# Optimization experiments

Hardware: AMD Instinct MI355X
Metric: run time of the kernel (lower is better)

## Reference

```python
import jax, jax.numpy as jnp
import numpy as np

B = 131072    # batch of toy 2D points
H = 256       # effective hidden width (dims[1], = out_dims * group_card)
NB = 8        # n_blocks i-ResBlocks
NMID = 3      # middle layers: dims 2->256->256->256->256->2 => 1 in + 3 mid + 1 out
NPS = 5       # n_power_series terms for log-det trace estimator


def setup_inputs() -> dict:
    key = jax.random.key(0)
    ks = jax.random.split(key, 8)
    # small scales keep each g-net contractive (coeff<1 Lipschitz, as spectral norm would)
    x  = jax.random.normal(ks[0], (B, 2), jnp.float32)
    v  = jax.random.normal(ks[1], (B, 2), jnp.float32)  # Hutchinson probe (n_samples=1)
    Wi = jax.random.normal(ks[2], (NB, 2, H), jnp.float32) * 0.05
    bi = jax.random.normal(ks[3], (NB, H), jnp.float32) * 0.01
    Wm = jax.random.normal(ks[4], (NB, NMID, H, H), jnp.float32) * (0.05 / np.sqrt(H))
    bm = jax.random.normal(ks[5], (NB, NMID, H), jnp.float32) * 0.01
    Wo = jax.random.normal(ks[6], (NB, H, 2), jnp.float32) * (0.05 / np.sqrt(H))
    bo = jax.random.normal(ks[7], (NB, 2), jnp.float32) * 0.01
    return {"x": x, "v": v, "Wi": Wi, "bi": bi, "Wm": Wm, "bm": bm, "Wo": Wo, "bo": bo}


def _g(x, Wi, bi, Wm, bm, Wo, bo):
    # equivariant 3x3 convs on 1x1 spatial maps == channel-mixing linears;
    # build_nnet appends the activation after EVERY conv, including the last.
    h = jax.nn.relu(x @ Wi + bi)
    for j in range(Wm.shape[0]):
        h = jax.nn.relu(h @ Wm[j] + bm[j])
    return jax.nn.relu(h @ Wo + bo)


def _iresblock(x, v, Wi, bi, Wm, bm, Wo, bo):
    gfun = lambda xx: _g(xx, Wi, bi, Wm, bm, Wo, bo)
    gx = gfun(x)
    # log det(I + J_g) ~= sum_{k=1..n} (-1)^{k+1}/k * v^T J_g^k v  (power series, Hutchinson)
    w = v
    logdet = jnp.zeros((x.shape[0], 1), x.dtype)
    for k in range(1, NPS + 1):
        _, w = jax.jvp(gfun, (x,), (w,))          # w <- J_g @ w
        coef = ((-1.0) ** (k + 1)) / k
        logdet = logdet + coef * jnp.sum(w * v, axis=1, keepdims=True)
    return x + gx, logdet


def reference(x, v, Wi, bi, Wm, bm, Wo, bo):
    z = x
    delta_logp = jnp.zeros((x.shape[0], 1), x.dtype)  # SequentialFlow: logpx - logdet per block
    for b in range(NB):
        z, ld = _iresblock(z, v, Wi[b], bi[b], Wm[b], bm[b], Wo[b], bo[b])
        delta_logp = delta_logp - ld
    return z, delta_logp
```

## Files before the change

### kernel.cpp

```cpp
#include <hip/hip_runtime.h>
#include <hip/hip_bf16.h>

#define BATCH 131072
#define H 256
#define NBLK 8
#define NMID 3
#define MS 16
#define RT_N 3
#define NT 256
#define CT_N 4

typedef __attribute__((ext_vector_type(8))) short short8;
typedef __attribute__((ext_vector_type(4))) float f32x4;

__device__ __forceinline__ unsigned pk2(float a, float b) {
    unsigned ua = __float_as_uint(a) + 0x8000u;
    unsigned ub = __float_as_uint(b) + 0x8000u;
    return __builtin_amdgcn_perm(ub, ua, 0x07060302u);
}

__global__ void pack_w_kernel(const float* __restrict__ Wm, unsigned short* __restrict__ Wp) {
    int o = blockIdx.x * blockDim.x + threadIdx.x;
    if (o >= NBLK * NMID * 8192) return;
    int lane  = o & 63;
    int T     = (o >> 6) & 15;
    int kk    = (o >> 10) & 7;
    int layer = o >> 13;
    int n  = (T >> 2) * 64 + (T & 1) * 32 + (lane & 15) * 2 + ((T >> 1) & 1);
    int k0 = kk * 32 + (lane >> 4) * 8;
    const float* src = Wm + (size_t)layer * H * H;
    unsigned int w[4];
    #pragma unroll
    for (int jj = 0; jj < 4; ++jj)
        w[jj] = pk2(src[(size_t)(k0 + 2*jj) * H + n], src[(size_t)(k0 + 2*jj + 1) * H + n]);
    uint4 val; val.x = w[0]; val.y = w[1]; val.z = w[2]; val.w = w[3];
    ((uint4*)Wp)[o] = val;
}

struct Packs { unsigned ph[4][2]; unsigned pa[4][2]; unsigned pb[4][2]; };

__device__ __forceinline__ void epi_compute(const f32x4 (&acc)[RT_N][CT_N],
                                            const float2 bvA, const float2 bvB, Packs& p) {
    #pragma unroll
    for (int r = 0; r < 4; ++r) {
        float a0 = acc[0][0][r] + bvA.x, a1 = acc[0][2][r] + bvA.y;
        float b0 = acc[0][1][r] + bvB.x, b1 = acc[0][3][r] + bvB.y;
        bool ma0 = a0 > 0.f, ma1 = a1 > 0.f, mb0 = b0 > 0.f, mb1 = b1 > 0.f;
        p.ph[r][0] = pk2(ma0 ? a0 : 0.f,            ma1 ? a1 : 0.f);
        p.ph[r][1] = pk2(mb0 ? b0 : 0.f,            mb1 ? b1 : 0.f);
        p.pa[r][0] = pk2(ma0 ? acc[1][0][r] : 0.f,  ma1 ? acc[1][2][r] : 0.f);
        p.pa[r][1] = pk2(mb0 ? acc[1][1][r] : 0.f,  mb1 ? acc[1][3][r] : 0.f);
        p.pb[r][0] = pk2(ma0 ? acc[2][0][r] : 0.f,  ma1 ? acc[2][2][r] : 0.f);
        p.pb[r][1] = pk2(mb0 ? acc[2][1][r] : 0.f,  mb1 ? acc[2][3][r] : 0.f);
    }
}

__device__ __forceinline__ void epi_store(const Packs& p, unsigned short* __restrict__ Xs,
                                          int wave, int lane) {
    const int mcol = lane & 15, quad = lane >> 4;
    const int qx = mcol >> 2;
    const int jb = (mcol & 3) * 2;
    const int kkA = wave * 2;
    #pragma unroll
    for (int r = 0; r < 4; ++r) {
        int le  = qx * 16 + quad * 4 + r;
        int scl = le ^ ((le >> 3) & 7);
        int e0  = kkA * 512 + scl * 8 + jb;
        *(unsigned*)(Xs + e0)               = p.ph[r][0];
        *(unsigned*)(Xs + e0 + 512)         = p.ph[r][1];
        *(unsigned*)(Xs + e0 + 4096)        = p.pa[r][0];
        *(unsigned*)(Xs + e0 + 4096 + 512)  = p.pa[r][1];
        *(unsigned*)(Xs + e0 + 8192)        = p.pb[r][0];
        *(unsigned*)(Xs + e0 + 8192 + 512)  = p.pb[r][1];
    }
}

__global__ __launch_bounds__(NT, 3)
void flow_kernel(const float* __restrict__ x, const float* __restrict__ v,
                 const float* __restrict__ Wi, const float* __restrict__ bi,
                 const float* __restrict__ bm, const float* __restrict__ Wo,
                 const float* __restrict__ bo,
                 const unsigned short* __restrict__ Wp,
                 float* __restrict__ out)
{
    __shared__ uint4 Xl4[RT_N * 8 * 64];
    __shared__ float zbuf[MS * 2];
    __shared__ float vbuf[MS * 2];

    unsigned short* Xs = (unsigned short*)Xl4;

    const int tid  = threadIdx.x;
    const int wave = tid >> 6;
    const int lane = tid & 63;
    const int mcol = lane & 15;
    const int quad = lane >> 4;
    const int s0   = blockIdx.x * MS;
    const int rl   = lane ^ ((lane >> 3) & 7);

    float dlp = 0.0f;
    if (tid < MS) {
        zbuf[tid*2+0] = x[(size_t)(s0+tid)*2+0];
        zbuf[tid*2+1] = x[(size_t)(s0+tid)*2+1];
        vbuf[tid*2+0] = v[(size_t)(s0+tid)*2+0];
        vbuf[tid*2+1] = v[(size_t)(s0+tid)*2+1];
    }
    __syncthreads();

    const int cA = wave * 64 + mcol * 2;

    for (int b = 0; b < NBLK; ++b) {
        {
            const float* Wi0 = Wi + (size_t)b * 2 * H;
            const float* Wi1 = Wi0 + H;
            short8 b0[CT_N];
            #pragma unroll
            for (int ct = 0; ct < CT_N; ++ct) {
                short8 z = {0,0,0,0,0,0,0,0};
                if (quad == 0) {
                    int n = cA + (ct & 1) * 32 + (ct >> 1);
                    unsigned p = pk2(Wi0[n], Wi1[n]);
                    z[0] = (short)(p & 0xFFFFu);
                    z[1] = (short)(p >> 16);
                }
                b0[ct] = z;
            }
            f32x4 acc[RT_N][CT_N];
            #pragma unroll
            for (int st = 0; st < RT_N; ++st)
                #pragma unroll
                for (int ct = 0; ct < CT_N; ++ct)
                    acc[st][ct] = (f32x4){0.f, 0.f, 0.f, 0.f};
            #pragma unroll
            for (int st = 0; st < RT_N; ++st) {
                short8 af = {0,0,0,0,0,0,0,0};
                if (quad == 0) {
                    if (st == 0) {
                        unsigned p = pk2(zbuf[mcol*2+0], zbuf[mcol*2+1]);
                        af[0] = (short)(p & 0xFFFFu);
                        af[1] = (short)(p >> 16);
                    } else if (st == 1) af[0] = (short)0x3F80;
                    else                af[1] = (short)0x3F80;
                }
                #pragma unroll
                for (int ct = 0; ct < CT_N; ++ct)
                    acc[st][ct] = __builtin_amdgcn_mfma_f32_16x16x32_bf16(af, b0[ct], acc[st][ct], 0, 0, 0);
            }
            Packs p;
            const float* bib = bi + (size_t)b * H;
            epi_compute(acc, *(const float2*)(bib + cA), *(const float2*)(bib + cA + 32), p);
            epi_store(p, Xs, wave, lane);
            __syncthreads();
        }

        for (int li = 0; li < NMID; ++li) {
            const int layer = b * NMID + li;
            const short8* Bp = ((const short8*)Wp) + (size_t)layer * 8192;

            f32x4 acc[RT_N][CT_N];
            #pragma unroll
            for (int st = 0; st < RT_N; ++st)
                #pragma unroll
                for (int ct = 0; ct < CT_N; ++ct)
                    acc[st][ct] = (f32x4){0.f, 0.f, 0.f, 0.f};

            #pragma unroll
            for (int kk = 0; kk < 8; ++kk) {
                short8 bf[CT_N];
                #pragma unroll
                for (int ct = 0; ct < CT_N; ++ct)
                    bf[ct] = Bp[(kk*16 + wave*4 + ct)*64 + lane];
                #pragma unroll
                for (int st = 0; st < RT_N; ++st) {
                    short8 af = ((const short8*)Xl4)[(st*8 + kk)*64 + rl];
                    #pragma unroll
                    for (int ct = 0; ct < CT_N; ++ct)
                        acc[st][ct] = __builtin_amdgcn_mfma_f32_16x16x32_bf16(af, bf[ct], acc[st][ct], 0, 0, 0);
                }
            }
            Packs p;
            const float* bmb = bm + (size_t)layer * H;
            epi_compute(acc, *(const float2*)(bmb + cA), *(const float2*)(bmb + cA + 32), p);
            __syncthreads();
            epi_store(p, Xs, wave, lane);
            __syncthreads();
        }

        {
            const float* Wob = Wo + (size_t)b * H * 2;
            const float* bob = bo + (size_t)b * 2;
            short8 b4[2];
            #pragma unroll
            for (int kki = 0; kki < 2; ++kki) {
                short8 z = {0,0,0,0,0,0,0,0};
                if (mcol < 2) {
                    int kb = (wave * 2 + kki) * 32 + quad * 8;
                    #pragma unroll
                    for (int jj = 0; jj < 4; ++jj) {
                        unsigned p = pk2(Wob[(kb + 2*jj) * 2 + mcol], Wob[(kb + 2*jj + 1) * 2 + mcol]);
                        z[2*jj]   = (short)(p & 0xFFFFu);
                        z[2*jj+1] = (short)(p >> 16);
                    }
                }
                b4[kki] = z;
            }
            f32x4 accL[RT_N];
            #pragma unroll
            for (int st = 0; st < RT_N; ++st) accL[st] = (f32x4){0.f, 0.f, 0.f, 0.f};
            #pragma unroll
            for (int st = 0; st < RT_N; ++st) {
                #pragma unroll
                for (int kki = 0; kki < 2; ++kki) {
                    short8 af = ((const short8*)Xl4)[(st*8 + wave*2 + kki)*64 + rl];
                    accL[st] = __builtin_amdgcn_mfma_f32_16x16x32_bf16(af, b4[kki], accL[st], 0, 0, 0);
                }
            }
            __syncthreads();
            float* part = (float*)Xl4;
            if (mcol < 2) {
                #pragma unroll
                for (int st = 0; st < RT_N; ++st)
                    #pragma unroll
                    for (int r = 0; r < 4; ++r)
                        part[((st*16 + quad*4 + r)*2 + mcol)*4 + wave] = accL[st][r];
            }
            __syncthreads();
            float* res = part + 384;
            if (tid < 96) {
                float4 p4 = ((const float4*)part)[tid];
                res[tid] = p4.x + p4.y + p4.z + p4.w;
            }
            __syncthreads();
            if (tid < MS) {
                float SH0 = res[tid*2],      SH1 = res[tid*2+1];
                float SA0 = res[32 + tid*2], SA1 = res[33 + tid*2];
                float SB0 = res[64 + tid*2], SB1 = res[65 + tid*2];
                float pre0 = SH0 + bob[0], pre1 = SH1 + bob[1];
                bool  m0 = pre0 > 0.f,     m1 = pre1 > 0.f;
                float gx0 = m0 ? pre0 : 0.f, gx1 = m1 ? pre1 : 0.f;
                float J00 = m0 ? SA0 : 0.f;
                float J01 = m0 ? SB0 : 0.f;
                float J10 = m1 ? SA1 : 0.f;
                float J11 = m1 ? SB1 : 0.f;
                float v0 = vbuf[tid*2+0], v1 = vbuf[tid*2+1];
                float w0 = v0, w1 = v1, ld = 0.f;
                const float coef[5] = {1.f, -0.5f, 1.f/3.f, -0.25f, 0.2f};
                #pragma unroll
                for (int k = 0; k < 5; ++k) {
                    float nw0 = fmaf(J00, w0, J01 * w1);
                    float nw1 = fmaf(J10, w0, J11 * w1);
                    w0 = nw0; w1 = nw1;
                    ld = fmaf(coef[k], fmaf(w0, v0, w1 * v1), ld);
                }
                zbuf[tid*2+0] += gx0;
                zbuf[tid*2+1] += gx1;
                dlp -= ld;
            }
            __syncthreads();
        }
    }

    if (tid < MS) {
        out[(size_t)(s0+tid)*2+0] = zbuf[tid*2+0];
        out[(size_t)(s0+tid)*2+1] = zbuf[tid*2+1];
        out[(size_t)2*BATCH + s0 + tid] = dlp;
    }
}

extern "C" void kernel_launch(void* const* d_in, const int* in_sizes, int n_in,
                              void* d_out, int out_size, void* d_ws, size_t ws_size,
                              hipStream_t stream) {
    const float* x  = (const float*)d_in[0];
    const float* v  = (const float*)d_in[1];
    const float* Wi = (const float*)d_in[2];
    const float* bi = (const float*)d_in[3];
    const float* Wm = (const float*)d_in[4];
    const float* bm = (const float*)d_in[5];
    const float* Wo = (const float*)d_in[6];
    const float* bo = (const float*)d_in[7];
    unsigned short* Wp = (unsigned short*)d_ws;

    int nchunks = NBLK * NMID * 8192;
    pack_w_kernel<<<(nchunks + 255) / 256, 256, 0, stream>>>(Wm, Wp);
    flow_kernel<<<BATCH / MS, NT, 0, stream>>>(x, v, Wi, bi, bm, Wo, bo, Wp, (float*)d_out);
}
```

Before: 1.262 ms.

## Double-buffer activations in LDS and prefetch weight fragments across k-steps and layers

Activation tiles now sit in two ping-pong LDS buffers, so each middle layer writes its output to the other buffer. This drops the barrier that used to separate the reads of one layer from the writes of the next. Weight B-fragments are software-pipelined two k-steps ahead, and the next layer's first fragments are prefetched during the current layer's tail, including before the input layer. __syncthreads is replaced by a raw lgkmcnt-wait plus s_barrier, and launch bounds drop from 3 to 2 blocks per SIMD to make room for the extra registers and LDS, at the cost of occupancy.

New measurement: 1.374 ms. 8.8% more time.

```diff
diff --git a/kernel.cpp b/kernel.cpp
--- a/kernel.cpp
+++ b/kernel.cpp
@@ -12,6 +12,10 @@
 
 typedef __attribute__((ext_vector_type(8))) short short8;
 typedef __attribute__((ext_vector_type(4))) float f32x4;
+
+__device__ __forceinline__ void barrier_lgkm() {
+    asm volatile("s_waitcnt lgkmcnt(0)\n\ts_barrier" ::: "memory");
+}
 
 __device__ __forceinline__ unsigned pk2(float a, float b) {
     unsigned ua = __float_as_uint(a) + 0x8000u;
@@ -75,7 +79,7 @@
     }
 }
 
-__global__ __launch_bounds__(NT, 3)
+__global__ __launch_bounds__(NT, 2)
 void flow_kernel(const float* __restrict__ x, const float* __restrict__ v,
                  const float* __restrict__ Wi, const float* __restrict__ bi,
                  const float* __restrict__ bm, const float* __restrict__ Wo,
@@ -83,11 +87,9 @@
                  const unsigned short* __restrict__ Wp,
                  float* __restrict__ out)
 {
-    __shared__ uint4 Xl4[RT_N * 8 * 64];
+    __shared__ uint4 Xbuf[2][RT_N * 8 * 64];
     __shared__ float zbuf[MS * 2];
     __shared__ float vbuf[MS * 2];
-
-    unsigned short* Xs = (unsigned short*)Xl4;
 
     const int tid  = threadIdx.x;
     const int wave = tid >> 6;
@@ -109,7 +111,17 @@
     const int cA = wave * 64 + mcol * 2;
 
     for (int b = 0; b < NBLK; ++b) {
+        const short8* Bp_base = ((const short8*)Wp) + (size_t)(b * NMID) * 8192;
+        short8 bf[2][CT_N];
+
         {
+            #pragma unroll
+            for (int ct = 0; ct < CT_N; ++ct)
+                bf[0][ct] = Bp_base[(0*16 + wave*4 + ct)*64 + lane];
+            #pragma unroll
+            for (int ct = 0; ct < CT_N; ++ct)
+                bf[1][ct] = Bp_base[(1*16 + wave*4 + ct)*64 + lane];
+
             const float* Wi0 = Wi + (size_t)b * 2 * H;
             const float* Wi1 = Wi0 + H;
             short8 b0[CT_N];
@@ -148,13 +160,15 @@
             Packs p;
             const float* bib = bi + (size_t)b * H;
             epi_compute(acc, *(const float2*)(bib + cA), *(const float2*)(bib + cA + 32), p);
-            epi_store(p, Xs, wave, lane);
-            __syncthreads();
+            epi_store(p, (unsigned short*)Xbuf[0], wave, lane);
+            barrier_lgkm();
         }
 
+        #pragma unroll
         for (int li = 0; li < NMID; ++li) {
-            const int layer = b * NMID + li;
-            const short8* Bp = ((const short8*)Wp) + (size_t)layer * 8192;
+            const int rb = li & 1, wb = rb ^ 1;
+            const short8* Bp = Bp_base + (size_t)li * 8192;
+            const short8* Bn = Bp + 8192;
 
             f32x4 acc[RT_N][CT_N];
             #pragma unroll
@@ -165,24 +179,28 @@
 
             #pragma unroll
             for (int kk = 0; kk < 8; ++kk) {
-                short8 bf[CT_N];
-                #pragma unroll
-                for (int ct = 0; ct < CT_N; ++ct)
-                    bf[ct] = Bp[(kk*16 + wave*4 + ct)*64 + lane];
                 #pragma unroll
                 for (int st = 0; st < RT_N; ++st) {
-                    short8 af = ((const short8*)Xl4)[(st*8 + kk)*64 + rl];
+                    short8 af = ((const short8*)Xbuf[rb])[(st*8 + kk)*64 + rl];
                     #pragma unroll
                     for (int ct = 0; ct < CT_N; ++ct)
-                        acc[st][ct] = __builtin_amdgcn_mfma_f32_16x16x32_bf16(af, bf[ct], acc[st][ct], 0, 0, 0);
+                        acc[st][ct] = __builtin_amdgcn_mfma_f32_16x16x32_bf16(af, bf[kk & 1][ct], acc[st][ct], 0, 0, 0);
+                }
+                if (kk < 6) {
+                    #pragma unroll
+                    for (int ct = 0; ct < CT_N; ++ct)
+                        bf[kk & 1][ct] = Bp[((kk+2)*16 + wave*4 + ct)*64 + lane];
+                } else if (li < NMID - 1) {
+                    #pragma unroll
+                    for (int ct = 0; ct < CT_N; ++ct)
+                        bf[kk & 1][ct] = Bn[((kk-6)*16 + wave*4 + ct)*64 + lane];
                 }
             }
             Packs p;
-            const float* bmb = bm + (size_t)layer * H;
+            const float* bmb = bm + (size_t)(b * NMID + li) * H;
             epi_compute(acc, *(const float2*)(bmb + cA), *(const float2*)(bmb + cA + 32), p);
-            __syncthreads();
-            epi_store(p, Xs, wave, lane);
-            __syncthreads();
+            epi_store(p, (unsigned short*)Xbuf[wb], wave, lane);
+            barrier_lgkm();
         }
 
         {
@@ -210,12 +228,11 @@
             for (int st = 0; st < RT_N; ++st) {
                 #pragma unroll
                 for (int kki = 0; kki < 2; ++kki) {
-                    short8 af = ((const short8*)Xl4)[(st*8 + wave*2 + kki)*64 + rl];
+                    short8 af = ((const short8*)Xbuf[1])[(st*8 + wave*2 + kki)*64 + rl];
                     accL[st] = __builtin_amdgcn_mfma_f32_16x16x32_bf16(af, b4[kki], accL[st], 0, 0, 0);
                 }
             }
-            __syncthreads();
-            float* part = (float*)Xl4;
+            float* part = (float*)Xbuf[0];
             if (mcol < 2) {
                 #pragma unroll
                 for (int st = 0; st < RT_N; ++st)
@@ -223,13 +240,13 @@
                     for (int r = 0; r < 4; ++r)
                         part[((st*16 + quad*4 + r)*2 + mcol)*4 + wave] = accL[st][r];
             }
-            __syncthreads();
+            barrier_lgkm();
             float* res = part + 384;
             if (tid < 96) {
                 float4 p4 = ((const float4*)part)[tid];
                 res[tid] = p4.x + p4.y + p4.z + p4.w;
             }
-            __syncthreads();
+            barrier_lgkm();
             if (tid < MS) {
                 float SH0 = res[tid*2],      SH1 = res[tid*2+1];
                 float SA0 = res[32 + tid*2], SA1 = res[33 + tid*2];
@@ -255,7 +272,7 @@
                 zbuf[tid*2+1] += gx1;
                 dlp -= ld;
             }
-            __syncthreads();
+            barrier_lgkm();
         }
     }
 
```
